# Optimization experiments

Hardware: AMD Instinct MI355X
Metric: run time of the kernel (lower is better)

Reference implementation:

```python
import jax, jax.numpy as jnp
import numpy as np

N, NFEAT, NHID, NREL, NCLASS, NHEADS = 4096, 512, 64, 64, 16, 8
ALPHA = 0.2   # LeakyReLU negative slope
NEG = -9e15   # pyGAT mask value


def _gat_layer(x, rel, mask, adj_ad, W, a1, a2, concat):
    # x: [N, Fin], rel: [nrel, Fin], mask: [N, N] bool, adj_ad: [N, nrel]
    xr = x + adj_ad @ rel                 # relation-augmented node features
    h = xr @ W                            # [N, Fout]
    f1 = h @ a1                           # [N]  (a^T[Wh_i||Wh_j] = f1_i + f2_j)
    f2 = h @ a2                           # [N]
    e = jax.nn.leaky_relu(f1[:, None] + f2[None, :], ALPHA)  # [N, N]
    att = jax.nn.softmax(jnp.where(mask, e, NEG), axis=1)
    out = att @ h                         # [N, Fout]
    return jax.nn.elu(out) if concat else out


def setup_inputs() -> dict:
    key = jax.random.key(0)
    ks = jax.random.split(key, 12)
    x = jax.random.normal(ks[0], (N, NFEAT), jnp.float32)
    rel = jax.random.normal(ks[1], (NREL, NFEAT), jnp.float32)
    rel_dict = jax.random.randint(ks[2], (N,), 0, NREL, jnp.int32)
    adj = (jax.random.uniform(ks[3], (N, N)) < 0.01).astype(jnp.float32)
    adj = jnp.maximum(adj, jnp.eye(N, dtype=jnp.float32))  # self loops
    adj_ad = jax.random.uniform(ks[4], (N, NREL), jnp.float32)
    adj_ad = adj_ad / adj_ad.sum(axis=1, keepdims=True)
    s_in = 1.0 / np.sqrt(NFEAT)
    s_hid = 1.0 / np.sqrt(NHID)
    s_cat = 1.0 / np.sqrt(NHID * NHEADS)
    W_heads = jax.random.normal(ks[5], (NHEADS, NFEAT, NHID), jnp.float32) * s_in
    a1_heads = jax.random.normal(ks[6], (NHEADS, NHID), jnp.float32) * s_hid
    a2_heads = jax.random.normal(ks[7], (NHEADS, NHID), jnp.float32) * s_hid
    W_out = jax.random.normal(ks[8], (NHID * NHEADS, NFEAT), jnp.float32) * s_cat
    a1_out = jax.random.normal(ks[9], (NFEAT,), jnp.float32) * s_in
    a2_out = jax.random.normal(ks[10], (NFEAT,), jnp.float32) * s_in
    lin_W = jax.random.normal(ks[11], (NFEAT, NCLASS), jnp.float32) * s_in
    lin_b = jnp.zeros((NCLASS,), jnp.float32)
    return {"x": x, "rel": rel, "rel_dict": rel_dict, "adj": adj, "adj_ad": adj_ad,
            "W_heads": W_heads, "a1_heads": a1_heads, "a2_heads": a2_heads,
            "W_out": W_out, "a1_out": a1_out, "a2_out": a2_out,
            "lin_W": lin_W, "lin_b": lin_b}


def reference(x, rel, rel_dict, adj, adj_ad, W_heads, a1_heads, a2_heads,
              W_out, a1_out, a2_out, lin_W, lin_b):
    # dropout is identity at inference (training=False); rel_dict is only used
    # by the repo to build adj/adj_ad, so it is a non-math constant here.
    mask = adj > 0
    # multi-head GAT layer, heads fused via vmap then concatenated on feature dim
    heads = jax.vmap(lambda W, a1, a2: _gat_layer(x, rel, mask, adj_ad, W, a1, a2, True))(
        W_heads, a1_heads, a2_heads)                      # [H, N, NHID]
    hcat = jnp.moveaxis(heads, 0, 1).reshape(N, NHEADS * NHID)  # [N, H*NHID]
    h2 = _gat_layer(hcat, rel, mask, adj_ad, W_out, a1_out, a2_out, False)  # [N, NFEAT]
    logits = jax.nn.elu(h2 @ lin_W + lin_b)               # [N, NCLASS]
    return jax.nn.log_softmax(logits, axis=1)
```

## Files before the change

### kernel.cpp

```cpp
#include <hip/hip_runtime.h>

#define NN      4096
#define FEAT    512
#define KDIM    576
#define NHID    64
#define NHEADS  8
#define NCLS    16
#define MAXDEG  128
#define ALPHA   0.2f

typedef __bf16 bf16_t;
typedef __bf16 bf16x8_t __attribute__((ext_vector_type(8)));
typedef float  f32x4_t  __attribute__((ext_vector_type(4)));
typedef unsigned short us8_t __attribute__((ext_vector_type(8)));

__device__ inline unsigned short f2bf(float f) {
    unsigned int u = __float_as_uint(f);
    u += 0x7fffu + ((u >> 16) & 1u);
    return (unsigned short)(u >> 16);
}
__device__ inline float bfu2f(unsigned short b) {
    return __uint_as_float(((unsigned int)b) << 16);
}

__global__ __launch_bounds__(256) void prep_kernel(
    const float* __restrict__ adj, int* __restrict__ deg, int* __restrict__ cols,
    const float* __restrict__ adj_ad, const float* __restrict__ rel,
    const float* __restrict__ x, bf16_t* __restrict__ Abf,
    bf16_t* __restrict__ Abf2,
    const float* __restrict__ Wh, const float* __restrict__ Wo,
    unsigned short* __restrict__ WcT, unsigned short* __restrict__ WoT,
    float* __restrict__ f1o, float* __restrict__ f2o) {
    int b = blockIdx.x;
    int t = threadIdx.x;
    __shared__ int wsum[4];
    __shared__ float srow[512];
    if (b < NN) {
        const float4* row4 = (const float4*)(adj + (size_t)b * NN);
        float4 v0 = row4[t];
        float4 v1 = row4[t + 256];
        float4 v2 = row4[t + 512];
        float4 v3 = row4[t + 768];
        unsigned mask = 0;
        mask |= (v0.x > 0.0f) << 0;  mask |= (v0.y > 0.0f) << 1;
        mask |= (v0.z > 0.0f) << 2;  mask |= (v0.w > 0.0f) << 3;
        mask |= (v1.x > 0.0f) << 4;  mask |= (v1.y > 0.0f) << 5;
        mask |= (v1.z > 0.0f) << 6;  mask |= (v1.w > 0.0f) << 7;
        mask |= (v2.x > 0.0f) << 8;  mask |= (v2.y > 0.0f) << 9;
        mask |= (v2.z > 0.0f) << 10; mask |= (v2.w > 0.0f) << 11;
        mask |= (v3.x > 0.0f) << 12; mask |= (v3.y > 0.0f) << 13;
        mask |= (v3.z > 0.0f) << 14; mask |= (v3.w > 0.0f) << 15;
        int c = __popc(mask);
        int lane = t & 63;
        int pre = c;
        #pragma unroll
        for (int off = 1; off < 64; off <<= 1) {
            int n = __shfl_up(pre, off);
            if (lane >= off) pre += n;
        }
        if (lane == 63) wsum[t >> 6] = pre;
        __syncthreads();
        int base = pre - c;
        #pragma unroll
        for (int w2 = 0; w2 < 4; ++w2)
            if (w2 < (t >> 6)) base += wsum[w2];
        int* colrow = cols + b * MAXDEG;
        unsigned mm = mask;
        int idx = base;
        while (mm) {
            int bit = __ffs(mm) - 1;
            mm &= mm - 1;
            int j = 4 * t + (bit >> 2) * 1024 + (bit & 3);
            if (idx < MAXDEG) colrow[idx] = j;
            ++idx;
        }
        if (t == 0) {
            int tot = wsum[0] + wsum[1] + wsum[2] + wsum[3];
            deg[b] = tot > MAXDEG ? MAXDEG : tot;
        }
    } else if (b < NN + 2048) {
        int half = t >> 7;
        int tt = t & 127;
        size_t i = (size_t)(b - NN) * 2 + half;
        float4 xv = ((const float4*)(x + i * FEAT))[tt];
        ushort4 o;
        o.x = f2bf(xv.x); o.y = f2bf(xv.y);
        o.z = f2bf(xv.z); o.w = f2bf(xv.w);
        *(ushort4*)(Abf + i * KDIM + 4 * tt) = o;
        if (tt < 16) {
            float4 av = ((const float4*)(adj_ad + i * 64))[tt];
            ushort4 o2;
            o2.x = f2bf(av.x); o2.y = f2bf(av.y);
            o2.z = f2bf(av.z); o2.w = f2bf(av.w);
            *(ushort4*)(Abf  + i * KDIM + 512 + 4 * tt) = o2;
            *(ushort4*)(Abf2 + i * KDIM + 512 + 4 * tt) = o2;
        }
    } else if (b < NN + 2048 + 2052) {
        int gid = (b - NN - 2048) * 256 + t;
        if (gid < 262144) {
            int n = gid >> 9, k = gid & 511;
            int h = n >> 6, f = n & 63;
            WcT[(size_t)n * KDIM + k] = f2bf(Wh[(h * 512 + k) * 64 + f]);
        } else if (gid < 524288) {
            int idx = gid - 262144;
            int n = idx >> 9, k = idx & 511;
            WoT[(size_t)n * KDIM + k] = f2bf(Wo[k * 512 + n]);
        } else {
            int idx = gid - 524288;
            ((float4*)f1o)[idx] = make_float4(0.f, 0.f, 0.f, 0.f);
            ((float4*)f2o)[idx] = make_float4(0.f, 0.f, 0.f, 0.f);
        }
    } else {
        int rb = b - NN - 2048 - 2052;
        int r  = rb & 63;
        int nh = (rb >> 6) & 1;
        int n  = nh * 256 + t;
        srow[t]       = rel[r * FEAT + t];
        srow[t + 256] = rel[r * FEAT + 256 + t];
        __syncthreads();
        float acc = 0.0f;
        if (rb < 128) {
            int h = n >> 6, f = n & 63;
            const float* p = Wh + (size_t)h * 32768 + f;
            #pragma unroll 4
            for (int k = 0; k < 512; ++k) acc += srow[k] * p[(size_t)k * 64];
            WcT[(size_t)n * KDIM + 512 + r] = f2bf(acc);
        } else {
            const float* p = Wo + n;
            #pragma unroll 4
            for (int k = 0; k < 512; ++k) acc += srow[k] * p[(size_t)k * 512];
            WoT[(size_t)n * KDIM + 512 + r] = f2bf(acc);
        }
    }
}

__global__ __launch_bounds__(256) void gemm_bf16_dot_kernel(
    const bf16_t* __restrict__ A, const bf16_t* __restrict__ Bt,
    unsigned short* __restrict__ Cbf,
    const float* __restrict__ a1, const float* __restrict__ a2,
    float* __restrict__ f1, float* __restrict__ f2, int layer2) {
    __shared__ __align__(16) bf16_t As[64][72];
    __shared__ __align__(16) bf16_t Bs[64][72];
    const int bm = blockIdx.x * 64;
    const int bn = blockIdx.y * 64;
    const int t  = threadIdx.x;
    const int lr = t >> 3;
    const int lc = (t & 7) * 8;
    const int l  = t & 63;
    const int w  = t >> 6;
    const int mrow = w * 16 + (l & 15);
    const int nrow = l & 15;
    const int q8 = (l >> 4) * 8;

    const bf16_t* Ap0 = A  + (size_t)(bm + lr)      * KDIM + lc;
    const bf16_t* Ap1 = A  + (size_t)(bm + 32 + lr) * KDIM + lc;
    const bf16_t* Bp0 = Bt + (size_t)(bn + lr)      * KDIM + lc;
    const bf16_t* Bp1 = Bt + (size_t)(bn + 32 + lr) * KDIM + lc;
    uint4 ra0 = *(const uint4*)(Ap0);
    uint4 ra1 = *(const uint4*)(Ap1);
    uint4 rb0 = *(const uint4*)(Bp0);
    uint4 rb1 = *(const uint4*)(Bp1);

    f32x4_t acc[4] = {};
    for (int k0 = 0; k0 < KDIM; k0 += 64) {
        *(uint4*)&As[lr][lc]      = ra0;
        *(uint4*)&As[32 + lr][lc] = ra1;
        *(uint4*)&Bs[lr][lc]      = rb0;
        *(uint4*)&Bs[32 + lr][lc] = rb1;
        __syncthreads();
        if (k0 + 64 < KDIM) {
            ra0 = *(const uint4*)(Ap0 + k0 + 64);
            ra1 = *(const uint4*)(Ap1 + k0 + 64);
            rb0 = *(const uint4*)(Bp0 + k0 + 64);
            rb1 = *(const uint4*)(Bp1 + k0 + 64);
        }
        #pragma unroll
        for (int kk = 0; kk < 64; kk += 32) {
            bf16x8_t a = *(const bf16x8_t*)&As[mrow][kk + q8];
            #pragma unroll
            for (int nt = 0; nt < 4; ++nt) {
                bf16x8_t b = *(const bf16x8_t*)&Bs[nt * 16 + nrow][kk + q8];
                acc[nt] = __builtin_amdgcn_mfma_f32_16x16x32_bf16(a, b, acc[nt], 0, 0, 0);
            }
        }
        __syncthreads();
    }
    const int crow = bm + w * 16 + (l >> 4) * 4;
    const int ccol = bn + (l & 15);
    #pragma unroll
    for (int nt = 0; nt < 4; ++nt)
        #pragma unroll
        for (int r = 0; r < 4; ++r)
            Cbf[(size_t)(crow + r) * FEAT + ccol + nt * 16] = f2bf(acc[nt][r]);

    float a1v[4], a2v[4];
    #pragma unroll
    for (int nt = 0; nt < 4; ++nt) {
        a1v[nt] = a1[bn + (l & 15) + nt * 16];
        a2v[nt] = a2[bn + (l & 15) + nt * 16];
    }
    float p1[4] = {}, p2[4] = {};
    #pragma unroll
    for (int nt = 0; nt < 4; ++nt)
        #pragma unroll
        for (int r = 0; r < 4; ++r) {
            p1[r] += acc[nt][r] * a1v[nt];
            p2[r] += acc[nt][r] * a2v[nt];
        }
    #pragma unroll
    for (int off = 1; off <= 8; off <<= 1)
        #pragma unroll
        for (int r = 0; r < 4; ++r) {
            p1[r] += __shfl_xor(p1[r], off);
            p2[r] += __shfl_xor(p2[r], off);
        }
    if ((l & 15) == 0) {
        int row = bm + w * 16 + (l >> 4) * 4;
        if (layer2) {
            #pragma unroll
            for (int r = 0; r < 4; ++r) {
                atomicAdd(&f1[row + r], p1[r]);
                atomicAdd(&f2[row + r], p2[r]);
            }
        } else {
            #pragma unroll
            for (int r = 0; r < 4; ++r) {
                f1[blockIdx.y * NN + row + r] = p1[r];
                f2[blockIdx.y * NN + row + r] = p2[r];
            }
        }
    }
}

__global__ __launch_bounds__(512) void att1_kernel(
    const bf16_t* __restrict__ Hbf, const float* __restrict__ f1,
    const float* __restrict__ f2, const int* __restrict__ deg,
    const int* __restrict__ cols, bf16_t* __restrict__ outbf) {
    int i = blockIdx.x;
    int tid = threadIdx.x;
    int h = tid >> 6;
    int l = tid & 63;
    __shared__ int jl[MAXDEG];
    __shared__ float se[NHEADS][MAXDEG];
    __shared__ float part[NHEADS][FEAT];
    __shared__ float sinv[NHEADS];
    __shared__ int sdeg;
    if (tid == 0) sdeg = deg[i];
    __syncthreads();
    int d = sdeg;
    int dpad = (d + 31) & ~31;
    for (int k = tid; k < dpad; k += 512)
        jl[k] = (k < d) ? cols[i * MAXDEG + k] : i;
    __syncthreads();
    float fi = f1[h * NN + i];
    float lmax = -1e30f;
    for (int k = l; k < d; k += 64) {
        float e = fi + f2[h * NN + jl[k]];
        e = e > 0.0f ? e : ALPHA * e;
        se[h][k] = e;
        lmax = fmaxf(lmax, e);
    }
    for (int off = 32; off; off >>= 1) lmax = fmaxf(lmax, __shfl_down(lmax, off));
    float m = __shfl(lmax, 0);
    float ls = 0.0f;
    for (int k = l; k < d; k += 64) {
        float p = __expf(se[h][k] - m);
        se[h][k] = p;
        ls += p;
    }
    for (int k = d + l; k < dpad; k += 64) se[h][k] = 0.0f;
    for (int off = 32; off; off >>= 1) ls += __shfl_down(ls, off);
    if (l == 0) sinv[h] = 1.0f / ls;
    __syncthreads();
    const int myhead = l >> 3;
    float acc[8] = {};
    for (int k0 = 0; k0 < dpad; k0 += 32) {
        float pw[4];
        const bf16_t* rp[4];
        #pragma unroll
        for (int j = 0; j < 4; ++j) {
            int k = k0 + j * 8 + h;
            pw[j] = se[myhead][k];
            rp[j] = Hbf + (size_t)jl[k] * FEAT + l * 8;
        }
        #pragma unroll
        for (int j = 0; j < 4; ++j) {
            us8_t v = *(const us8_t*)rp[j];
            float p = pw[j];
            #pragma unroll
            for (int q = 0; q < 8; ++q) acc[q] += p * bfu2f(v[q]);
        }
    }
    *(float4*)&part[h][l * 8]     = make_float4(acc[0], acc[1], acc[2], acc[3]);
    *(float4*)&part[h][l * 8 + 4] = make_float4(acc[4], acc[5], acc[6], acc[7]);
    __syncthreads();
    {
        float sum = 0.0f;
        #pragma unroll
        for (int w2 = 0; w2 < NHEADS; ++w2) sum += part[w2][tid];
        float o = sum * sinv[tid >> 6];
        o = o > 0.0f ? o : __expf(o) - 1.0f;
        ((unsigned short*)outbf)[(size_t)i * KDIM + tid] = f2bf(o);
    }
}

__global__ __launch_bounds__(256) void att2_final_kernel(
    const bf16_t* __restrict__ Hbf, const float* __restrict__ f1,
    const float* __restrict__ f2, const int* __restrict__ deg,
    const int* __restrict__ cols, const float* __restrict__ linW,
    const float* __restrict__ linb, float* __restrict__ out) {
    int i = blockIdx.x;
    int t = threadIdx.x;
    __shared__ int jl[MAXDEG];
    __shared__ float sp[MAXDEG];
    __shared__ float red[4];
    __shared__ float part[3][FEAT];
    __shared__ float hrow[FEAT];
    __shared__ float clsred[16][NCLS];
    __shared__ float sl[NCLS];
    __shared__ int sdeg;
    if (t == 0) sdeg = deg[i];
    __syncthreads();
    int d = sdeg;
    int dpad = (d + 15) & ~15;
    if (t < dpad) jl[t] = (t < d) ? cols[i * MAXDEG + t] : i;
    __syncthreads();
    float e = 0.0f, lmax = -1e30f;
    if (t < d) {
        e = f1[i] + f2[jl[t]];
        e = e > 0.0f ? e : ALPHA * e;
        lmax = e;
    }
    for (int off = 32; off; off >>= 1) lmax = fmaxf(lmax, __shfl_down(lmax, off));
    if ((t & 63) == 0) red[t >> 6] = lmax;
    __syncthreads();
    float m = fmaxf(fmaxf(red[0], red[1]), fmaxf(red[2], red[3]));
    float p = 0.0f;
    if (t < d) p = __expf(e - m);
    if (t < dpad) sp[t] = p;
    float ls = p;
    for (int off = 32; off; off >>= 1) ls += __shfl_down(ls, off);
    __syncthreads();
    if ((t & 63) == 0) red[t >> 6] = ls;
    __syncthreads();
    float s = red[0] + red[1] + red[2] + red[3];
    float inv = 1.0f / s;
    const int slot = t >> 6;
    const int cg   = t & 63;
    float acc[8] = {};
    for (int k0 = 0; k0 < dpad; k0 += 16) {
        float pw[4];
        const bf16_t* rp[4];
        #pragma unroll
        for (int j = 0; j < 4; ++j) {
            int k = k0 + j * 4 + slot;
            pw[j] = sp[k];
            rp[j] = Hbf + (size_t)jl[k] * FEAT + cg * 8;
        }
        #pragma unroll
        for (int j = 0; j < 4; ++j) {
            us8_t v = *(const us8_t*)rp[j];
            float pk = pw[j];
            #pragma unroll
            for (int q = 0; q < 8; ++q) acc[q] += pk * bfu2f(v[q]);
        }
    }
    if (slot > 0) {
        float* dst = &part[slot - 1][cg * 8];
        *(float4*)(dst)     = make_float4(acc[0], acc[1], acc[2], acc[3]);
        *(float4*)(dst + 4) = make_float4(acc[4], acc[5], acc[6], acc[7]);
    }
    __syncthreads();
    if (slot == 0) {
        #pragma unroll
        for (int sl2 = 0; sl2 < 3; ++sl2)
            #pragma unroll
            for (int j = 0; j < 8; ++j) acc[j] += part[sl2][cg * 8 + j];
        float* dst = &hrow[cg * 8];
        *(float4*)(dst)     = make_float4(acc[0] * inv, acc[1] * inv, acc[2] * inv, acc[3] * inv);
        *(float4*)(dst + 4) = make_float4(acc[4] * inv, acc[5] * inv, acc[6] * inv, acc[7] * inv);
    }
    __syncthreads();
    {
        int c = t & 15;
        int seg = t >> 4;
        float partial = 0.0f;
        int f0 = seg * 32;
        #pragma unroll 8
        for (int f = f0; f < f0 + 32; ++f) partial += hrow[f] * linW[f * NCLS + c];
        clsred[seg][c] = partial;
    }
    __syncthreads();
    if (t < NCLS) {
        float logit = linb[t];
        #pragma unroll
        for (int seg = 0; seg < 16; ++seg) logit += clsred[seg][t];
        logit = logit > 0.0f ? logit : __expf(logit) - 1.0f;
        sl[t] = logit;
    }
    __syncthreads();
    if (t < NCLS) {
        float mm = sl[0];
        #pragma unroll
        for (int c = 1; c < NCLS; ++c) mm = fmaxf(mm, sl[c]);
        float ssum = 0.0f;
        #pragma unroll
        for (int c = 0; c < NCLS; ++c) ssum += __expf(sl[c] - mm);
        out[i * NCLS + t] = sl[t] - mm - logf(ssum);
    }
}

extern "C" void kernel_launch(void* const* d_in, const int* in_sizes, int n_in,
                              void* d_out, int out_size, void* d_ws, size_t ws_size,
                              hipStream_t stream) {
    const float* x        = (const float*)d_in[0];
    const float* rel      = (const float*)d_in[1];
    const float* adj      = (const float*)d_in[3];
    const float* adj_ad   = (const float*)d_in[4];
    const float* W_heads  = (const float*)d_in[5];
    const float* a1_heads = (const float*)d_in[6];
    const float* a2_heads = (const float*)d_in[7];
    const float* W_out    = (const float*)d_in[8];
    const float* a1_out   = (const float*)d_in[9];
    const float* a2_out   = (const float*)d_in[10];
    const float* lin_W    = (const float*)d_in[11];
    const float* lin_b    = (const float*)d_in[12];
    float* out = (float*)d_out;

    char* ws = (char*)d_ws;
    bf16_t* Abf  = (bf16_t*)(ws);
    bf16_t* Abf2 = (bf16_t*)(ws + (5u  << 20));
    bf16_t* Hbf1 = (bf16_t*)(ws + (10u << 20));
    bf16_t* Hbf2 = (bf16_t*)(ws + (14u << 20));
    bf16_t* WcT  = (bf16_t*)(ws + (18u << 20));
    bf16_t* WoT  = (bf16_t*)(ws + (19u << 20));
    float*  f1   = (float*) (ws + (20u << 20));
    float*  f2   = (float*) (ws + (20u << 20) + (128u << 10));
    float*  f1o  = (float*) (ws + (20u << 20) + (256u << 10));
    float*  f2o  = (float*) (ws + (20u << 20) + (272u << 10));
    int*    deg  = (int*)   (ws + (20u << 20) + (288u << 10));
    int*    cols = (int*)   (ws + (21u << 20));

    prep_kernel<<<NN + 2048 + 2052 + 256, 256, 0, stream>>>(
        adj, deg, cols, adj_ad, rel, x, Abf, Abf2, W_heads, W_out,
        (unsigned short*)WcT, (unsigned short*)WoT, f1o, f2o);
    gemm_bf16_dot_kernel<<<dim3(64, 8), 256, 0, stream>>>(
        Abf, WcT, (unsigned short*)Hbf1, a1_heads, a2_heads, f1, f2, 0);
    att1_kernel<<<NN, 512, 0, stream>>>(Hbf1, f1, f2, deg, cols, Abf2);
    gemm_bf16_dot_kernel<<<dim3(64, 8), 256, 0, stream>>>(
        Abf2, WoT, (unsigned short*)Hbf2, a1_out, a2_out, f1o, f2o, 1);
    att2_final_kernel<<<NN, 256, 0, stream>>>(Hbf2, f1o, f2o, deg, cols, lin_W, lin_b, out);
}
```

Before: 207.1 us.

## Restructure prep kernel: coalesced weight transposes, wave-per-row CSR, reordered block roles

Reorganizes the fused prep kernel. The serial rel@W dot-product blocks now run first, with eight independent accumulators, so the long-latency tail starts early. The scattered per-element weight transposes become 64x64 tiles staged through padded shared memory, giving coalesced reads and writes. The adjacency-to-CSR pass now uses one wavefront per row with 64-bit masks, so it no longer needs a block-level scan or barrier. Together this cuts the block count and strided global accesses, at the cost of more registers per thread in the CSR path and a changed float summation order for the relation projection.

```diff
diff --git a/kernel.cpp b/kernel.cpp
--- a/kernel.cpp
+++ b/kernel.cpp
@@ -22,6 +22,13 @@
 __device__ inline float bfu2f(unsigned short b) {
     return __uint_as_float(((unsigned int)b) << 16);
 }
+
+#define PREP_REL0   0
+#define PREP_TR0    256
+#define PREP_Z0     384
+#define PREP_CAST0  392
+#define PREP_CSR0   2440
+#define PREP_NBLK   3464
 
 __global__ __launch_bounds__(256) void prep_kernel(
     const float* __restrict__ adj, int* __restrict__ deg, int* __restrict__ cols,
@@ -33,55 +40,79 @@
     float* __restrict__ f1o, float* __restrict__ f2o) {
     int b = blockIdx.x;
     int t = threadIdx.x;
-    __shared__ int wsum[4];
-    __shared__ float srow[512];
-    if (b < NN) {
-        const float4* row4 = (const float4*)(adj + (size_t)b * NN);
-        float4 v0 = row4[t];
-        float4 v1 = row4[t + 256];
-        float4 v2 = row4[t + 512];
-        float4 v3 = row4[t + 768];
-        unsigned mask = 0;
-        mask |= (v0.x > 0.0f) << 0;  mask |= (v0.y > 0.0f) << 1;
-        mask |= (v0.z > 0.0f) << 2;  mask |= (v0.w > 0.0f) << 3;
-        mask |= (v1.x > 0.0f) << 4;  mask |= (v1.y > 0.0f) << 5;
-        mask |= (v1.z > 0.0f) << 6;  mask |= (v1.w > 0.0f) << 7;
-        mask |= (v2.x > 0.0f) << 8;  mask |= (v2.y > 0.0f) << 9;
-        mask |= (v2.z > 0.0f) << 10; mask |= (v2.w > 0.0f) << 11;
-        mask |= (v3.x > 0.0f) << 12; mask |= (v3.y > 0.0f) << 13;
-        mask |= (v3.z > 0.0f) << 14; mask |= (v3.w > 0.0f) << 15;
-        int c = __popc(mask);
-        int lane = t & 63;
-        int pre = c;
-        #pragma unroll
-        for (int off = 1; off < 64; off <<= 1) {
-            int n = __shfl_up(pre, off);
-            if (lane >= off) pre += n;
-        }
-        if (lane == 63) wsum[t >> 6] = pre;
+    __shared__ float smem[64 * 65];
+    if (b < PREP_TR0) {
+        int r  = b & 63;
+        int nh = (b >> 6) & 1;
+        int n  = nh * 256 + t;
+        smem[t]       = rel[r * FEAT + t];
+        smem[t + 256] = rel[r * FEAT + 256 + t];
         __syncthreads();
-        int base = pre - c;
-        #pragma unroll
-        for (int w2 = 0; w2 < 4; ++w2)
-            if (w2 < (t >> 6)) base += wsum[w2];
-        int* colrow = cols + b * MAXDEG;
-        unsigned mm = mask;
-        int idx = base;
-        while (mm) {
-            int bit = __ffs(mm) - 1;
-            mm &= mm - 1;
-            int j = 4 * t + (bit >> 2) * 1024 + (bit & 3);
-            if (idx < MAXDEG) colrow[idx] = j;
-            ++idx;
-        }
-        if (t == 0) {
-            int tot = wsum[0] + wsum[1] + wsum[2] + wsum[3];
-            deg[b] = tot > MAXDEG ? MAXDEG : tot;
-        }
-    } else if (b < NN + 2048) {
+        float acc[8] = {};
+        if (b < 128) {
+            int h = n >> 6, f = n & 63;
+            const float* p = Wh + (size_t)h * 32768 + f;
+            for (int k0 = 0; k0 < 512; k0 += 8)
+                #pragma unroll
+                for (int u = 0; u < 8; ++u)
+                    acc[u] += smem[k0 + u] * p[(size_t)(k0 + u) * 64];
+            float s = ((acc[0] + acc[1]) + (acc[2] + acc[3]))
+                    + ((acc[4] + acc[5]) + (acc[6] + acc[7]));
+            WcT[(size_t)n * KDIM + 512 + r] = f2bf(s);
+        } else {
+            const float* p = Wo + n;
+            for (int k0 = 0; k0 < 512; k0 += 8)
+                #pragma unroll
+                for (int u = 0; u < 8; ++u)
+                    acc[u] += smem[k0 + u] * p[(size_t)(k0 + u) * 512];
+            float s = ((acc[0] + acc[1]) + (acc[2] + acc[3]))
+                    + ((acc[4] + acc[5]) + (acc[6] + acc[7]));
+            WoT[(size_t)n * KDIM + 512 + r] = f2bf(s);
+        }
+    } else if (b < PREP_Z0) {
+        int tb = b - PREP_TR0;
+        if (tb < 64) {
+            int h = tb >> 3, k0 = (tb & 7) * 64;
+            const float* src = Wh + (size_t)h * 32768 + (size_t)k0 * 64;
+            #pragma unroll
+            for (int i2 = 0; i2 < 16; ++i2) {
+                int li = t + i2 * 256;
+                float v = src[li];
+                smem[(li & 63) * 65 + (li >> 6)] = v;
+            }
+            __syncthreads();
+            #pragma unroll
+            for (int i2 = 0; i2 < 16; ++i2) {
+                int li = t + i2 * 256;
+                int f = li >> 6, r = li & 63;
+                WcT[(size_t)(h * 64 + f) * KDIM + k0 + r] = f2bf(smem[f * 65 + r]);
+            }
+        } else {
+            int wb = tb - 64;
+            int n0 = (wb & 7) * 64, k0 = (wb >> 3) * 64;
+            #pragma unroll
+            for (int i2 = 0; i2 < 16; ++i2) {
+                int li = t + i2 * 256;
+                int r = li >> 6, f = li & 63;
+                float v = Wo[(size_t)(k0 + r) * 512 + n0 + f];
+                smem[f * 65 + r] = v;
+            }
+            __syncthreads();
+            #pragma unroll
+            for (int i2 = 0; i2 < 16; ++i2) {
+                int li = t + i2 * 256;
+                int f = li >> 6, r = li & 63;
+                WoT[(size_t)(n0 + f) * KDIM + k0 + r] = f2bf(smem[f * 65 + r]);
+            }
+        }
+    } else if (b < PREP_CAST0) {
+        int g = (b - PREP_Z0) * 256 + t;
+        if (g < 1024) ((float4*)f1o)[g] = make_float4(0.f, 0.f, 0.f, 0.f);
+        else ((float4*)f2o)[g - 1024] = make_float4(0.f, 0.f, 0.f, 0.f);
+    } else if (b < PREP_CSR0) {
         int half = t >> 7;
         int tt = t & 127;
-        size_t i = (size_t)(b - NN) * 2 + half;
+        size_t i = (size_t)(b - PREP_CAST0) * 2 + half;
         float4 xv = ((const float4*)(x + i * FEAT))[tt];
         ushort4 o;
         o.x = f2bf(xv.x); o.y = f2bf(xv.y);
@@ -95,41 +126,39 @@
             *(ushort4*)(Abf  + i * KDIM + 512 + 4 * tt) = o2;
             *(ushort4*)(Abf2 + i * KDIM + 512 + 4 * tt) = o2;
         }
-    } else if (b < NN + 2048 + 2052) {
-        int gid = (b - NN - 2048) * 256 + t;
-        if (gid < 262144) {
-            int n = gid >> 9, k = gid & 511;
-            int h = n >> 6, f = n & 63;
-            WcT[(size_t)n * KDIM + k] = f2bf(Wh[(h * 512 + k) * 64 + f]);
-        } else if (gid < 524288) {
-            int idx = gid - 262144;
-            int n = idx >> 9, k = idx & 511;
-            WoT[(size_t)n * KDIM + k] = f2bf(Wo[k * 512 + n]);
-        } else {
-            int idx = gid - 524288;
-            ((float4*)f1o)[idx] = make_float4(0.f, 0.f, 0.f, 0.f);
-            ((float4*)f2o)[idx] = make_float4(0.f, 0.f, 0.f, 0.f);
-        }
     } else {
-        int rb = b - NN - 2048 - 2052;
-        int r  = rb & 63;
-        int nh = (rb >> 6) & 1;
-        int n  = nh * 256 + t;
-        srow[t]       = rel[r * FEAT + t];
-        srow[t + 256] = rel[r * FEAT + 256 + t];
-        __syncthreads();
-        float acc = 0.0f;
-        if (rb < 128) {
-            int h = n >> 6, f = n & 63;
-            const float* p = Wh + (size_t)h * 32768 + f;
-            #pragma unroll 4
-            for (int k = 0; k < 512; ++k) acc += srow[k] * p[(size_t)k * 64];
-            WcT[(size_t)n * KDIM + 512 + r] = f2bf(acc);
-        } else {
-            const float* p = Wo + n;
-            #pragma unroll 4
-            for (int k = 0; k < 512; ++k) acc += srow[k] * p[(size_t)k * 512];
-            WoT[(size_t)n * KDIM + 512 + r] = f2bf(acc);
+        int l = t & 63;
+        int i = (b - PREP_CSR0) * 4 + (t >> 6);
+        const float4* row4 = (const float4*)(adj + (size_t)i * NN);
+        float4 v[16];
+        #pragma unroll
+        for (int c2 = 0; c2 < 16; ++c2) v[c2] = row4[l + c2 * 64];
+        unsigned long long mask = 0;
+        #pragma unroll
+        for (int c2 = 0; c2 < 16; ++c2) {
+            unsigned m4 = (unsigned)(v[c2].x > 0.0f)
+                        | ((unsigned)(v[c2].y > 0.0f) << 1)
+                        | ((unsigned)(v[c2].z > 0.0f) << 2)
+                        | ((unsigned)(v[c2].w > 0.0f) << 3);
+            mask |= (unsigned long long)m4 << (4 * c2);
+        }
+        int c = __popcll(mask);
+        int pre = c;
+        #pragma unroll
+        for (int off = 1; off < 64; off <<= 1) {
+            int n = __shfl_up(pre, off);
+            if (l >= off) pre += n;
+        }
+        int base = pre - c;
+        if (l == 63) deg[i] = pre > MAXDEG ? MAXDEG : pre;
+        int* colrow = cols + i * MAXDEG;
+        int idx = base;
+        while (mask) {
+            int bit = (int)__ffsll(mask) - 1;
+            mask &= mask - 1;
+            int j = 4 * l + ((bit >> 2) << 8) + (bit & 3);
+            if (idx < MAXDEG) colrow[idx] = j;
+            ++idx;
         }
     }
 }
@@ -441,7 +470,7 @@
     int*    deg  = (int*)   (ws + (20u << 20) + (288u << 10));
     int*    cols = (int*)   (ws + (21u << 20));
 
-    prep_kernel<<<NN + 2048 + 2052 + 256, 256, 0, stream>>>(
+    prep_kernel<<<PREP_NBLK, 256, 0, stream>>>(
         adj, deg, cols, adj_ad, rel, x, Abf, Abf2, W_heads, W_out,
         (unsigned short*)WcT, (unsigned short*)WoT, f1o, f2o);
     gemm_bf16_dot_kernel<<<dim3(64, 8), 256, 0, stream>>>(
```

After: 188.4 us. 1.1x faster.
